# Kernel optimization log

Hardware: AMD Instinct MI355X
Metric: run time of the kernel (lower is better)

## Reference

```python
import jax, jax.numpy as jnp
import numpy as np

N, E, F, HID, HEADS, L, OUT = 25000, 400000, 128, 128, 2, 3, 10
C = HID // HEADS
EPS = 1e-5

def _ln(x, g, b):
    m = jnp.mean(x, -1, keepdims=True)
    v = jnp.mean((x - m) ** 2, -1, keepdims=True)
    return (x - m) / jnp.sqrt(v + EPS) * g + b

def _lrelu(x, s=0.01):
    return jnp.where(x >= 0, x, s * x)

def setup_inputs():
    key = jax.random.key(0)
    ks = iter(jax.random.split(key, 80))
    def nrm(shape, fan_in):
        return jax.random.normal(next(ks), shape, dtype=jnp.float32) / np.float32(np.sqrt(fan_in))
    return {
        "x": jax.random.normal(next(ks), (N, F), dtype=jnp.float32),
        "edge_index": jax.random.randint(next(ks), (2, E), 0, N, dtype=jnp.int32),
        "edge_attr": jax.random.uniform(next(ks), (E,), dtype=jnp.float32),
        "task_features": jax.random.normal(next(ks), (4,), dtype=jnp.float32),
        "emb_w": nrm((F, HID), F), "emb_b": jnp.zeros((HID,), jnp.float32),
        "emb_g": jnp.ones((HID,), jnp.float32), "emb_beta": jnp.zeros((HID,), jnp.float32),
        "gat_w": nrm((L, HID, HID), HID),
        "gat_as": nrm((L, HEADS, C), C), "gat_ad": nrm((L, HEADS, C), C),
        "gat_bias": jnp.zeros((L, HID), jnp.float32),
        "ec_w1": nrm((L, 2 * HID, HID), 2 * HID), "ec_b1": jnp.zeros((L, HID), jnp.float32),
        "ec_g1": jnp.ones((L, HID), jnp.float32), "ec_be1": jnp.zeros((L, HID), jnp.float32),
        "ec_w2": nrm((L, HID, HID), HID), "ec_b2": jnp.zeros((L, HID), jnp.float32),
        "ec_g2": jnp.ones((L, HID), jnp.float32), "ec_be2": jnp.zeros((L, HID), jnp.float32),
        "norm_g": jnp.ones((L, HID), jnp.float32), "norm_b": jnp.zeros((L, HID), jnp.float32),
        "task_w": nrm((4, HID), 4), "task_b": jnp.zeros((HID,), jnp.float32),
        "task_g": jnp.ones((HID,), jnp.float32), "task_beta": jnp.zeros((HID,), jnp.float32),
        "pa_w1": nrm((HID, HID // 2), HID), "pa_b1": jnp.zeros((HID // 2,), jnp.float32),
        "pa_w2": nrm((HID // 2, 1), HID // 2), "pa_b2": jnp.zeros((1,), jnp.float32),
        "v_w1": nrm((2 * HID, HID), 2 * HID), "v_b1": jnp.zeros((HID,), jnp.float32),
        "v_g": jnp.ones((HID,), jnp.float32), "v_be": jnp.zeros((HID,), jnp.float32),
        "v_w2": nrm((HID, 1), HID), "v_b2": jnp.zeros((1,), jnp.float32),
        "a_w1": nrm((2 * HID, HID), 2 * HID), "a_b1": jnp.zeros((HID,), jnp.float32),
        "a_g": jnp.ones((HID,), jnp.float32), "a_be": jnp.zeros((HID,), jnp.float32),
        "a_w2": nrm((HID, OUT), HID), "a_b2": jnp.zeros((OUT,), jnp.float32),
    }

def _forward(x, edge_attr, task_features, emb_w, emb_b, emb_g, emb_beta,
             gat_w, gat_as, gat_ad, gat_bias,
             ec_w1, ec_b1, ec_g1, ec_be1, ec_w2, ec_b2, ec_g2, ec_be2,
             norm_g, norm_b, task_w, task_b, task_g, task_beta,
             pa_w1, pa_b1, pa_w2, pa_b2,
             v_w1, v_b1, v_g, v_be, v_w2, v_b2,
             a_w1, a_b1, a_g, a_be, a_w2, a_b2, edge_index):
    src, dst = edge_index[0], edge_index[1]
    loop = jnp.arange(N, dtype=edge_index.dtype)
    src_sl = jnp.concatenate([src, loop])  # PyG GATConv adds self-loops
    dst_sl = jnp.concatenate([dst, loop])
    h = _lrelu(_ln(x @ emb_w + emb_b, emb_g, emb_beta))
    x0 = h
    for i in range(L):
        # --- GATConv (dropout inactive at eval) ---
        ht = (h @ gat_w[i]).reshape(N, HEADS, C)
        a_s = jnp.sum(ht * gat_as[i], -1)  # [N, HEADS]
        a_d = jnp.sum(ht * gat_ad[i], -1)
        e = _lrelu(a_s[src_sl] + a_d[dst_sl], 0.2)  # [E+N, HEADS]
        emax = jax.ops.segment_max(e, dst_sl, num_segments=N)
        ee = jnp.exp(e - emax[dst_sl])
        alpha = ee / jax.ops.segment_sum(ee, dst_sl, num_segments=N)[dst_sl]
        x1 = jax.ops.segment_sum(ht[src_sl] * alpha[:, :, None], dst_sl,
                                 num_segments=N).reshape(N, HID) + gat_bias[i]
        # --- EdgeConv: gather -> MLP -> weighted scatter-add ---
        ef = jnp.concatenate([h[src], h[dst]], axis=1)  # [E, 2*HID]
        ef = _lrelu(_ln(ef @ ec_w1[i] + ec_b1[i], ec_g1[i], ec_be1[i]), 0.2)
        ef = _lrelu(_ln(ef @ ec_w2[i] + ec_b2[i], ec_g2[i], ec_be2[i]), 0.2)
        ef = ef * edge_attr[:, None]
        x2 = jax.ops.segment_sum(ef, dst, num_segments=N)
        h = _lrelu(_ln(x1 + x2, norm_g[i], norm_b[i]))
        if i > 0:
            h = h + x0
            x0 = h
    # attention pooling over all nodes (batch=None path)
    w = jax.nn.softmax((_lrelu(h @ pa_w1 + pa_b1) @ pa_w2 + pa_b2)[:, 0])
    gf = jnp.sum(h * w[:, None], axis=0)  # [HID]
    te = _lrelu(_ln(task_features @ task_w + task_b, task_g, task_beta))
    cf = jnp.concatenate([gf, te], -1)  # [2*HID]
    value = _lrelu(_ln(cf @ v_w1 + v_b1, v_g, v_be)) @ v_w2 + v_b2
    adv = _lrelu(_ln(cf @ a_w1 + a_b1, a_g, a_be)) @ a_w2 + a_b2
    return value + (adv - jnp.mean(adv, -1, keepdims=True))

def reference(x, edge_index, edge_attr, task_features, emb_w, emb_b, emb_g, emb_beta, gat_w, gat_as, gat_ad, gat_bias, ec_w1, ec_b1, ec_g1, ec_be1, ec_w2, ec_b2, ec_g2, ec_be2, norm_g, norm_b, task_w, task_b, task_g, task_beta, pa_w1, pa_b1, pa_w2, pa_b2, v_w1, v_b1, v_g, v_be, v_w2, v_b2, a_w1, a_b1, a_g, a_be, a_w2, a_b2):
    return _forward(x, edge_attr, task_features, emb_w, emb_b, emb_g, emb_beta, gat_w, gat_as, gat_ad, gat_bias, ec_w1, ec_b1, ec_g1, ec_be1, ec_w2, ec_b2, ec_g2, ec_be2, norm_g, norm_b, task_w, task_b, task_g, task_beta, pa_w1, pa_b1, pa_w2, pa_b2, v_w1, v_b1, v_g, v_be, v_w2, v_b2, a_w1, a_b1, a_g, a_be, a_w2, a_b2, edge_index)
```

## Files before the change

### kernel.cpp

```cpp
#include <hip/hip_runtime.h>
#include <math.h>

#define NN 25000
#define EE 400000
#define LL 3
#define LNEPS 1e-5f
#define EB 64

typedef __attribute__((ext_vector_type(8))) short short8;
typedef __attribute__((ext_vector_type(16))) float f32x16;

__device__ __forceinline__ float lrelu(float x, float s) { return fmaxf(x, x * s); }

__device__ __forceinline__ unsigned int pack_bf2(float lo, float hi) {
    unsigned int ul = __float_as_uint(lo), uh = __float_as_uint(hi);
    ul = (ul + 0x7FFFu + ((ul >> 16) & 1u)) >> 16;
    uh = (uh + 0x7FFFu + ((uh >> 16) & 1u)) >> 16;
    return (uh << 16) | (ul & 0xFFFFu);
}
__device__ __forceinline__ float bf_lo(unsigned int u) { return __uint_as_float(u << 16); }
__device__ __forceinline__ float bf_hi(unsigned int u) { return __uint_as_float(u & 0xFFFF0000u); }

__device__ __forceinline__ void ln_stats128(float v, float* red, float& mean, float& inv) {
    float sm = v, sq = v * v;
#pragma unroll
    for (int m = 32; m >= 1; m >>= 1) { sm += __shfl_xor(sm, m); sq += __shfl_xor(sq, m); }
    __syncthreads();
    if ((threadIdx.x & 63) == 0) { red[(threadIdx.x >> 6) * 2] = sm; red[(threadIdx.x >> 6) * 2 + 1] = sq; }
    __syncthreads();
    sm = red[0] + red[2]; sq = red[1] + red[3];
    mean = sm * (1.f / 128.f);
    float var = sq * (1.f / 128.f) - mean * mean;
    inv = rsqrtf(var + LNEPS);
}

__global__ void k_hist(const int* __restrict__ dst, int* __restrict__ cnt, int ne)
{
    int i = blockIdx.x * 256 + threadIdx.x;
    if (i < ne) atomicAdd(&cnt[dst[i]], 1);
}

__global__ __launch_bounds__(1024) void k_scan(const int* __restrict__ cnt,
                                               int* __restrict__ starts, int n)
{
    __shared__ int tot[1024];
    int t = threadIdx.x;
    const int PER = (n + 1023) >> 10;
    int i0 = t * PER;
    int s = 0;
    for (int k = 0; k < PER; ++k) { int i = i0 + k; s += (i < n) ? cnt[i] : 0; }
    tot[t] = s;
    __syncthreads();
    for (int off = 1; off < 1024; off <<= 1) {
        int x = (t >= off) ? tot[t - off] : 0;
        __syncthreads();
        tot[t] += x;
        __syncthreads();
    }
    int run = (t > 0) ? tot[t - 1] : 0;
    for (int k = 0; k < PER; ++k) {
        int i = i0 + k;
        if (i < n) { starts[i] = run; run += cnt[i]; }
    }
    if (t == 1023) starts[n] = tot[1023];
}

__global__ void k_scatter(const int* __restrict__ src, const int* __restrict__ dst,
                          const float* __restrict__ ea, int* __restrict__ cursor,
                          int* __restrict__ s_src, int* __restrict__ s_dst,
                          float* __restrict__ s_ea, int ne)
{
    int i = blockIdx.x * 256 + threadIdx.x;
    if (i >= ne) return;
    int d = dst[i];
    int pos = atomicAdd(&cursor[d], 1);
    s_src[pos] = src[i];
    s_dst[pos] = d;
    s_ea[pos] = ea[i];
}

__global__ void k_prep(const float* __restrict__ gat_w, const float* __restrict__ ec_w1,
                       const float* __restrict__ ec_w2, const float* __restrict__ emb_w,
                       uint4* __restrict__ wf)
{
    int g = blockIdx.x * 256 + threadIdx.x;
    int m = g >> 11, f = g & 2047;
    const float* srcm;
    if (m < 3) srcm = gat_w + (size_t)m * 16384;
    else if (m < 9) { int t2 = m - 3; srcm = ec_w1 + (size_t)(t2 >> 1) * 32768 + (size_t)(t2 & 1) * 16384; }
    else if (m < 12) srcm = ec_w2 + (size_t)(m - 9) * 16384;
    else srcm = emb_w;
    int l = f & 63, ks = (f >> 6) & 7, nb = f >> 9;
    int k0 = ks * 16 + (l >> 5) * 8, col = nb * 32 + (l & 31);
    const float* wp = srcm + (size_t)k0 * 128 + col;
    uint4 r;
    r.x = pack_bf2(wp[0],   wp[128]);
    r.y = pack_bf2(wp[256], wp[384]);
    r.z = pack_bf2(wp[512], wp[640]);
    r.w = pack_bf2(wp[768], wp[896]);
    wf[g] = r;
}

__global__ __launch_bounds__(256) void k_emb(
    const float* __restrict__ in, const uint4* __restrict__ wfm,
    const float* __restrict__ bias, const float* __restrict__ g,
    const float* __restrict__ be, float* __restrict__ h,
    float* __restrict__ x0, int nrows)
{
    __shared__ __align__(16) unsigned int sA[64 * 64];
    __shared__ __align__(16) unsigned int sW[2048 * 4];
    float* sU = (float*)sW;
    const int tid = threadIdx.x;
    const int r0 = blockIdx.x * 64;
    {
        int row = tid >> 2, q = tid & 3;
        const float* srcp = in + (size_t)(r0 + row) * 128 + q * 32;
        bool ok = (r0 + row) < nrows;
#pragma unroll
        for (int i = 0; i < 8; ++i) {
            float4 v = ok ? *(const float4*)&srcp[i * 4] : make_float4(0.f, 0.f, 0.f, 0.f);
            int cu = (q * 16 + i * 2) ^ ((row & 15) << 2);
            *(uint2*)&sA[row * 64 + cu] = make_uint2(pack_bf2(v.x, v.y), pack_bf2(v.z, v.w));
        }
    }
    {
        uint4* sW4 = (uint4*)sW;
#pragma unroll
        for (int i = 0; i < 8; ++i) sW4[tid + 256 * i] = wfm[tid + 256 * i];
    }
    __syncthreads();
    const int w = tid >> 6, l = tid & 63;
    const int m0 = (w >> 1) * 32, nhalf = (w & 1);
    f32x16 acc0 = {}, acc1 = {};
#pragma unroll
    for (int ks = 0; ks < 8; ++ks) {
        int rw = m0 + (l & 31);
        int cu = (ks * 8 + (l >> 5) * 4) ^ ((rw & 15) << 2);
        short8 a = *(const short8*)&sA[rw * 64 + cu];
        short8 b0 = *(const short8*)&sW[((nhalf * 16 + ks) * 64 + l) * 4];
        short8 b1 = *(const short8*)&sW[(((nhalf * 2 + 1) * 8 + ks) * 64 + l) * 4];
        acc0 = __builtin_amdgcn_mfma_f32_32x32x16_bf16(a, b0, acc0, 0, 0, 0);
        acc1 = __builtin_amdgcn_mfma_f32_32x32x16_bf16(a, b1, acc1, 0, 0, 0);
    }
    __syncthreads();
    {
        int colbase = nhalf * 64 + (l & 31);
        float bb0 = bias[colbase], bb1 = bias[colbase + 32];
#pragma unroll
        for (int r = 0; r < 16; ++r) {
            int rw = m0 + (r & 3) + 8 * (r >> 2) + 4 * (l >> 5);
            sU[rw * 128 + colbase]      = acc0[r] + bb0;
            sU[rw * 128 + colbase + 32] = acc1[r] + bb1;
        }
    }
    __syncthreads();
    float2 gv = *(const float2*)&g[l * 2];
    float2 bv = *(const float2*)&be[l * 2];
    for (int it = 0; it < 16; ++it) {
        int rw = w * 16 + it;
        int grow = r0 + rw;
        if (grow >= nrows) break;
        float2 v = *(const float2*)&sU[rw * 128 + l * 2];
        float sm = v.x + v.y, sq = v.x * v.x + v.y * v.y;
#pragma unroll
        for (int m = 32; m >= 1; m >>= 1) { sm += __shfl_xor(sm, m); sq += __shfl_xor(sq, m); }
        float mean = sm * (1.f / 128.f);
        float var = sq * (1.f / 128.f) - mean * mean;
        float inv = rsqrtf(var + LNEPS);
        float o0 = lrelu((v.x - mean) * inv * gv.x + bv.x, 0.01f);
        float o1 = lrelu((v.y - mean) * inv * gv.y + bv.y, 0.01f);
        unsigned off = (unsigned)grow * 128u + (unsigned)(l * 2);
        *(float2*)&h[off]  = make_float2(o0, o1);
        *(float2*)&x0[off] = make_float2(o0, o1);
    }
}

__global__ __launch_bounds__(256) void k_gemm3(
    const float* __restrict__ in, const uint4* __restrict__ wf,
    int mht, int mA, int mB, const float* __restrict__ bA,
    unsigned* __restrict__ o0, unsigned* __restrict__ o1, unsigned* __restrict__ o2,
    int nrows)
{
    __shared__ __align__(16) unsigned int sA[64 * 64];
    __shared__ __align__(16) unsigned int sW[2048 * 4];
    const int tid = threadIdx.x;
    const int r0 = blockIdx.x * 64;
    {
        int row = tid >> 2, q = tid & 3;
        const float* srcp = in + (size_t)(r0 + row) * 128 + q * 32;
        bool ok = (r0 + row) < nrows;
#pragma unroll
        for (int i = 0; i < 8; ++i) {
            float4 v = ok ? *(const float4*)&srcp[i * 4] : make_float4(0.f, 0.f, 0.f, 0.f);
            unsigned int p0 = pack_bf2(v.x, v.y), p1 = pack_bf2(v.z, v.w);
            int cu = (q * 16 + i * 2) ^ ((row & 15) << 2);
            *(uint2*)&sA[row * 64 + cu] = make_uint2(p0, p1);
        }
    }
    __syncthreads();
    const int w = tid >> 6, l = tid & 63;
    const int m0 = (w >> 1) * 32, nhalf = (w & 1);
    short8 af[8];
#pragma unroll
    for (int ks = 0; ks < 8; ++ks) {
        int row = m0 + (l & 31);
        int cu = (ks * 8 + (l >> 5) * 4) ^ ((row & 15) << 2);
        af[ks] = *(const short8*)&sA[row * 64 + cu];
    }
    const int c = l & 31;
    const bool evenl = (c & 1) == 0;
    const unsigned uidx = (unsigned)(nhalf * 32 + (evenl ? (c >> 1) : (16 + (c >> 1))));
    auto do_mat = [&](int mat, unsigned* out, const float* bp) {
        __syncthreads();
        {
            const uint4* wsrc = wf + (size_t)mat * 2048;
            uint4* sW4 = (uint4*)sW;
#pragma unroll
            for (int i = 0; i < 8; ++i) sW4[tid + 256 * i] = wsrc[tid + 256 * i];
        }
        __syncthreads();
        f32x16 acc0 = {}, acc1 = {};
        const int nb0 = nhalf * 2;
#pragma unroll
        for (int ks = 0; ks < 8; ++ks) {
            short8 b0 = *(const short8*)&sW[((nb0 * 8 + ks) * 64 + l) * 4];
            short8 b1v = *(const short8*)&sW[(((nb0 + 1) * 8 + ks) * 64 + l) * 4];
            acc0 = __builtin_amdgcn_mfma_f32_32x32x16_bf16(af[ks], b0, acc0, 0, 0, 0);
            acc1 = __builtin_amdgcn_mfma_f32_32x32x16_bf16(af[ks], b1v, acc1, 0, 0, 0);
        }
        int colbase = nhalf * 64 + c;
        float badd0 = bp ? bp[colbase] : 0.f;
        float badd1 = bp ? bp[colbase + 32] : 0.f;
#pragma unroll
        for (int r = 0; r < 16; ++r) {
            float v0 = acc0[r] + badd0;
            float v1 = acc1[r] + badd1;
            float v0p = __shfl_xor(v0, 1);
            float v1p = __shfl_xor(v1, 1);
            int row = r0 + m0 + (r & 3) + 8 * (r >> 2) + 4 * (l >> 5);
            if (row < nrows) {
                unsigned val = evenl ? pack_bf2(v0, v0p) : pack_bf2(v1p, v1);
                out[(unsigned)row * 64u + uidx] = val;
            }
        }
    };
    do_mat(mht, o0, nullptr);
    do_mat(mA, o1, bA);
    do_mat(mB, o2, nullptr);
}

__global__ __launch_bounds__(512) void k_node_scores(
    const unsigned* __restrict__ htp, const unsigned* __restrict__ Apk,
    const unsigned* __restrict__ Bpk,
    const float* __restrict__ as_, const float* __restrict__ ad_,
    float* __restrict__ a_s, float* __restrict__ a_d,
    float* __restrict__ denom, float* __restrict__ selfe,
    float* __restrict__ rsA, float* __restrict__ rsB, int n)
{
    int wv = threadIdx.x >> 6, ln = threadIdx.x & 63;
    int node = blockIdx.x * 8 + wv;
    if (node >= n) return;
    unsigned off = (unsigned)node * 64u + (unsigned)ln;
    unsigned hv = htp[off], av = Apk[off], bv = Bpk[off];
    float h0 = bf_lo(hv), h1 = bf_hi(hv);
    float2 wsv = *(const float2*)&as_[ln * 2];
    float2 wdv = *(const float2*)&ad_[ln * 2];
    float ss = h0 * wsv.x + h1 * wsv.y;
    float sd = h0 * wdv.x + h1 * wdv.y;
    float sa = bf_lo(av) + bf_hi(av), sb = bf_lo(bv) + bf_hi(bv);
#pragma unroll
    for (int m = 16; m >= 1; m >>= 1) {
        ss += __shfl_xor(ss, m); sd += __shfl_xor(sd, m);
        sa += __shfl_xor(sa, m); sb += __shfl_xor(sb, m);
    }
    float sa2 = sa + __shfl_xor(sa, 32);
    float sb2 = sb + __shfl_xor(sb, 32);
    if ((ln & 31) == 0) {
        int hd = ln >> 5;
        a_s[node * 2 + hd] = ss;
        a_d[node * 2 + hd] = sd;
        float ev = expf(lrelu(ss + sd, 0.2f));
        denom[node * 2 + hd] = ev;
        selfe[node * 2 + hd] = ev;
        if (hd == 0) { rsA[node] = sa2; rsB[node] = sb2; }
    }
}

__global__ void k_edge_denom2(const int* __restrict__ s_src, const int* __restrict__ s_dst,
                              const float* __restrict__ a_s, const float* __restrict__ a_d,
                              float* __restrict__ denom, float* __restrict__ expo,
                              float4* __restrict__ xz, int nz4, int ne)
{
    int gtid = blockIdx.x * 256 + threadIdx.x;
    for (int i = gtid; i < nz4; i += gridDim.x * 256)
        xz[i] = make_float4(0.f, 0.f, 0.f, 0.f);
    int base = gtid * 8;
    if (base >= ne) return;
    int curd = -1;
    float acc0 = 0.f, acc1 = 0.f;
    for (int k = 0; k < 8; ++k) {
        int e = base + k;
        if (e >= ne) break;
        int s = s_src[e], d = s_dst[e];
        float v0 = expf(lrelu(a_s[(unsigned)(s * 2)]     + a_d[(unsigned)(d * 2)],     0.2f));
        float v1 = expf(lrelu(a_s[(unsigned)(s * 2 + 1)] + a_d[(unsigned)(d * 2 + 1)], 0.2f));
        *(float2*)&expo[(unsigned)e * 2] = make_float2(v0, v1);
        if (d != curd) {
            if (curd >= 0) { atomicAdd(&denom[curd * 2], acc0); atomicAdd(&denom[curd * 2 + 1], acc1); }
            curd = d; acc0 = v0; acc1 = v1;
        } else { acc0 += v0; acc1 += v1; }
    }
    if (curd >= 0) { atomicAdd(&denom[curd * 2], acc0); atomicAdd(&denom[curd * 2 + 1], acc1); }
}

__global__ __launch_bounds__(512) void k_edge_main(
    const unsigned* __restrict__ Apk, const unsigned* __restrict__ Bpk,
    const unsigned* __restrict__ htp,
    const int* __restrict__ s_src, const int* __restrict__ s_dst,
    const float* __restrict__ s_ea,
    const float* __restrict__ expo, const float* __restrict__ denom,
    const uint4* __restrict__ w2f,
    const float* __restrict__ rsA, const float* __restrict__ rsB,
    const float* __restrict__ g1, const float* __restrict__ be1,
    const float* __restrict__ b2, const float* __restrict__ g2, const float* __restrict__ be2,
    float* __restrict__ xsum, int ne)
{
    __shared__ __align__(16) unsigned int sWB[2048 * 4];
    __shared__ __align__(16) unsigned int sT32[EB * 64];
    __shared__ int   sS[EB], sD[EB];
    __shared__ float sEA[EB], sM[EB];
    __shared__ float sAl[EB * 2];
    __shared__ float sMean[EB], sInv[EB];
    __shared__ float sG1[128], sE1[128], sB2[128], sG2[128], sE2[128];
    float* sU = (float*)sWB;

    const int tid = threadIdx.x;
    {
        uint4* sWB4 = (uint4*)sWB;
#pragma unroll
        for (int i = 0; i < 4; ++i) { int f = tid + 512 * i; sWB4[f] = w2f[f]; }
    }
    if (tid < 128) {
        sG1[tid] = g1[tid]; sE1[tid] = be1[tid];
        sB2[tid] = b2[tid]; sG2[tid] = g2[tid]; sE2[tid] = be2[tid];
    }
    const int e0 = blockIdx.x * EB;
    const int nev = (ne - e0 < EB) ? (ne - e0) : EB;
    if (tid < EB) {
        if (tid < nev) {
            int s = s_src[e0 + tid], d = s_dst[e0 + tid];
            sS[tid] = s; sD[tid] = d; sEA[tid] = s_ea[e0 + tid];
            sM[tid] = (rsA[s] + rsB[d]) * (1.f / 128.f);
        } else { sS[tid] = 0; sD[tid] = -1; sEA[tid] = 0.f; sM[tid] = 0.f; }
    }
    if (tid < 2 * EB) {
        int le = tid >> 1, hd = tid & 1;
        float al = 0.f;
        if (le < nev) {
            int e = e0 + le;
            int d = s_dst[e];
            al = expo[(unsigned)e * 2 + hd] / denom[(unsigned)(d * 2 + hd)];
        }
        sAl[le * 2 + hd] = al;
    }
    __syncthreads();

    const int wv = tid >> 6, ln = tid & 63;
    const int half = ln >> 5, lc = ln & 31;

    {
        const float g10 = sG1[lc * 4], g11 = sG1[lc * 4 + 1], g12 = sG1[lc * 4 + 2], g13 = sG1[lc * 4 + 3];
        const float e10 = sE1[lc * 4], e11 = sE1[lc * 4 + 1], e12 = sE1[lc * 4 + 2], e13 = sE1[lc * 4 + 3];
        for (int j = 0; j < 4; ++j) {
            int e = wv * 8 + j * 2 + half;
            if (e < nev) {
                unsigned s = (unsigned)sS[e], d = (unsigned)sD[e];
                float mean = sM[e];
                uint2 av = *(const uint2*)&Apk[s * 64u + (unsigned)(lc * 2)];
                uint2 bv = *(const uint2*)&Bpk[d * 64u + (unsigned)(lc * 2)];
                float v0 = bf_lo(av.x) + bf_lo(bv.x) - mean;
                float v1 = bf_hi(av.x) + bf_hi(bv.x) - mean;
                float v2 = bf_lo(av.y) + bf_lo(bv.y) - mean;
                float v3 = bf_hi(av.y) + bf_hi(bv.y) - mean;
                float sq = v0 * v0 + v1 * v1 + v2 * v2 + v3 * v3;
#pragma unroll
                for (int m = 16; m >= 1; m >>= 1) sq += __shfl_xor(sq, m);
                float inv = rsqrtf(sq * (1.f / 128.f) + LNEPS);
                float t0 = lrelu(v0 * inv * g10 + e10, 0.2f);
                float t1 = lrelu(v1 * inv * g11 + e11, 0.2f);
                float t2 = lrelu(v2 * inv * g12 + e12, 0.2f);
                float t3 = lrelu(v3 * inv * g13 + e13, 0.2f);
                int cu = (lc * 2) ^ ((e & 15) << 2);
                *(uint2*)&sT32[e * 64 + cu] = make_uint2(pack_bf2(t0, t1), pack_bf2(t2, t3));
            }
        }
    }
    __syncthreads();

    {
        const int w = wv, l = ln;
        const int m0 = (w >> 2) * 32, n0 = (w & 3) * 32;
        f32x16 acc = {};
#pragma unroll
        for (int ks = 0; ks < 8; ++ks) {
            int row = m0 + (l & 31);
            int colu = (ks * 8 + (l >> 5) * 4) ^ ((row & 15) << 2);
            short8 a = *(const short8*)&sT32[row * 64 + colu];
            short8 b = *(const short8*)&sWB[((((w & 3) * 8 + ks) * 64 + l)) * 4];
            acc = __builtin_amdgcn_mfma_f32_32x32x16_bf16(a, b, acc, 0, 0, 0);
        }
        __syncthreads();
        float b2c = sB2[n0 + (l & 31)];
#pragma unroll
        for (int r = 0; r < 16; ++r) {
            int row = m0 + (r & 3) + 8 * (r >> 2) + 4 * (l >> 5);
            sU[row * 128 + n0 + (l & 31)] = acc[r] + b2c;
        }
    }
    __syncthreads();

    for (int j = 0; j < 4; ++j) {
        int e = wv * 8 + j * 2 + half;
        if (e < nev) {
            float4 u = *(const float4*)&sU[e * 128 + lc * 4];
            float sm = u.x + u.y + u.z + u.w;
            float sq = u.x * u.x + u.y * u.y + u.z * u.z + u.w * u.w;
#pragma unroll
            for (int m = 16; m >= 1; m >>= 1) { sm += __shfl_xor(sm, m); sq += __shfl_xor(sq, m); }
            if (lc == 0) {
                float mean = sm * (1.f / 128.f);
                sMean[e] = mean;
                sInv[e] = rsqrtf(sq * (1.f / 128.f) - mean * mean + LNEPS);
            }
        }
    }

    {
        const unsigned ln2 = (unsigned)(ln * 2);
        const float g2a = sG2[ln * 2], g2b = sG2[ln * 2 + 1];
        const float e2a = sE2[ln * 2], e2b = sE2[ln * 2 + 1];
        int curd = -1;
        float acc0 = 0.f, acc1 = 0.f;
        for (int j = 0; j < 8; ++j) {
            int e = wv * 8 + j;
            if (e >= nev) break;
            unsigned s = (unsigned)sS[e];
            int d = sD[e];
            float mean = sMean[e], inv = sInv[e];
            float2 uv = *(const float2*)&sU[e * 128 + ln * 2];
            float eav = sEA[e];
            float v0 = lrelu((uv.x - mean) * inv * g2a + e2a, 0.2f) * eav;
            float v1 = lrelu((uv.y - mean) * inv * g2b + e2b, 0.2f) * eav;
            float al = sAl[e * 2 + half];
            unsigned hv = htp[s * 64u + ln];
            v0 += bf_lo(hv) * al;
            v1 += bf_hi(hv) * al;
            if (d != curd) {
                if (curd >= 0) {
                    atomicAdd(&xsum[(unsigned)curd * 128u + ln2], acc0);
                    atomicAdd(&xsum[(unsigned)curd * 128u + ln2 + 1], acc1);
                }
                curd = d; acc0 = v0; acc1 = v1;
            } else { acc0 += v0; acc1 += v1; }
        }
        if (curd >= 0) {
            atomicAdd(&xsum[(unsigned)curd * 128u + ln2], acc0);
            atomicAdd(&xsum[(unsigned)curd * 128u + ln2 + 1], acc1);
        }
    }
}

__global__ __launch_bounds__(512) void k_norm8(const float* __restrict__ xsum,
                                               const unsigned* __restrict__ htp,
                                               const float* __restrict__ selfe,
                                               const float* __restrict__ denom,
                                               const float* __restrict__ gbias,
                                               const float* __restrict__ g,
                                               const float* __restrict__ b,
                                               float* __restrict__ x0,
                                               float* __restrict__ h, int n, int layer)
{
    int wv = threadIdx.x >> 6, ln = threadIdx.x & 63;
    int node = blockIdx.x * 8 + wv;
    if (node >= n) return;
    unsigned off = (unsigned)node * 128u + (unsigned)(ln * 2);
    int hd = ln >> 5;
    float alpha = selfe[node * 2 + hd] / denom[node * 2 + hd];
    unsigned hv = htp[(unsigned)node * 64u + (unsigned)ln];
    float2 gb = *(const float2*)&gbias[ln * 2];
    float2 v = *(const float2*)&xsum[off];
    v.x += gb.x + bf_lo(hv) * alpha;
    v.y += gb.y + bf_hi(hv) * alpha;
    float sm = v.x + v.y, sq = v.x * v.x + v.y * v.y;
#pragma unroll
    for (int m = 32; m >= 1; m >>= 1) { sm += __shfl_xor(sm, m); sq += __shfl_xor(sq, m); }
    float mean = sm * (1.f / 128.f);
    float var = sq * (1.f / 128.f) - mean * mean;
    float inv = rsqrtf(var + LNEPS);
    float2 gv = *(const float2*)&g[ln * 2];
    float2 bv = *(const float2*)&b[ln * 2];
    float val0 = lrelu((v.x - mean) * inv * gv.x + bv.x, 0.01f);
    float val1 = lrelu((v.y - mean) * inv * gv.y + bv.y, 0.01f);
    if (layer > 0) {
        float2 x0v = *(const float2*)&x0[off];
        val0 += x0v.x; val1 += x0v.y;
        *(float2*)&x0[off] = make_float2(val0, val1);
    }
    *(float2*)&h[off] = make_float2(val0, val1);
}

__global__ __launch_bounds__(256) void k_pool_score(const float* __restrict__ h,
    const float* __restrict__ w1, const float* __restrict__ b1,
    const float* __restrict__ w2, const float* __restrict__ b2,
    float* __restrict__ score, int n)
{
    int wv = threadIdx.x >> 6, ln = threadIdx.x & 63;
    int node = blockIdx.x * 4 + wv;
    if (node >= n) return;
    float acc = b1[ln];
    const float* hr = h + (size_t)node * 128;
    for (int k = 0; k < 128; ++k) acc += hr[k] * w1[k * 64 + ln];
    acc = lrelu(acc, 0.01f) * w2[ln];
#pragma unroll
    for (int m = 32; m >= 1; m >>= 1) acc += __shfl_xor(acc, m);
    if (ln == 0) score[node] = acc + b2[0];
}

__global__ __launch_bounds__(256) void k_softmax_reduce(const float* __restrict__ score,
                                                        float* __restrict__ stats,
                                                        float* __restrict__ gf, int n)
{
    __shared__ float red[8];
    int t = threadIdx.x;
    float mx = -1e30f;
    for (int i = t; i < n; i += 256) mx = fmaxf(mx, score[i]);
#pragma unroll
    for (int m = 32; m >= 1; m >>= 1) mx = fmaxf(mx, __shfl_xor(mx, m));
    if ((t & 63) == 0) red[t >> 6] = mx;
    __syncthreads();
    mx = fmaxf(fmaxf(red[0], red[1]), fmaxf(red[2], red[3]));
    float s = 0.f;
    for (int i = t; i < n; i += 256) s += expf(score[i] - mx);
#pragma unroll
    for (int m = 32; m >= 1; m >>= 1) s += __shfl_xor(s, m);
    if ((t & 63) == 0) red[4 + (t >> 6)] = s;
    __syncthreads();
    s = red[4] + red[5] + red[6] + red[7];
    if (t == 0) { stats[0] = mx; stats[1] = s; }
    if (t < 128) gf[t] = 0.f;
}

__global__ __launch_bounds__(128) void k_gf(const float* __restrict__ h,
                                            const float* __restrict__ score,
                                            const float* __restrict__ stats,
                                            float* __restrict__ gf, int n)
{
    int c = threadIdx.x;
    float mx = stats[0], invZ = 1.f / stats[1];
    int per = (n + gridDim.x - 1) / gridDim.x;
    int n0 = blockIdx.x * per;
    int n1 = n0 + per; if (n1 > n) n1 = n;
    float acc = 0.f;
    for (int i = n0; i < n1; ++i)
        acc += expf(score[i] - mx) * invZ * h[(size_t)i * 128 + c];
    atomicAdd(&gf[c], acc);
}

__global__ __launch_bounds__(128) void k_head(
    const float* __restrict__ gf, const float* __restrict__ tf,
    const float* __restrict__ task_w, const float* __restrict__ task_b,
    const float* __restrict__ task_g, const float* __restrict__ task_be,
    const float* __restrict__ v_w1, const float* __restrict__ v_b1,
    const float* __restrict__ v_g, const float* __restrict__ v_be,
    const float* __restrict__ v_w2, const float* __restrict__ v_b2,
    const float* __restrict__ a_w1, const float* __restrict__ a_b1,
    const float* __restrict__ a_g, const float* __restrict__ a_be,
    const float* __restrict__ a_w2, const float* __restrict__ a_b2,
    float* __restrict__ out)
{
    __shared__ float cf[256], hbuf[128], red[4], sc[2], adv[10];
    int t = threadIdx.x;
    float mean, inv;
    float te = task_b[t];
#pragma unroll
    for (int k = 0; k < 4; ++k) te += tf[k] * task_w[k * 128 + t];
    ln_stats128(te, red, mean, inv);
    te = lrelu((te - mean) * inv * task_g[t] + task_be[t], 0.01f);
    cf[t] = gf[t]; cf[128 + t] = te;
    __syncthreads();
    float v = v_b1[t];
    for (int k = 0; k < 256; ++k) v += cf[k] * v_w1[k * 128 + t];
    ln_stats128(v, red, mean, inv);
    v = lrelu((v - mean) * inv * v_g[t] + v_be[t], 0.01f);
    float pv = v * v_w2[t];
#pragma unroll
    for (int m = 32; m >= 1; m >>= 1) pv += __shfl_xor(pv, m);
    __syncthreads();
    if ((t & 63) == 0) red[t >> 6] = pv;
    __syncthreads();
    if (t == 0) sc[0] = red[0] + red[1] + v_b2[0];
    float a = a_b1[t];
    for (int k = 0; k < 256; ++k) a += cf[k] * a_w1[k * 128 + t];
    ln_stats128(a, red, mean, inv);
    a = lrelu((a - mean) * inv * a_g[t] + a_be[t], 0.01f);
    hbuf[t] = a;
    __syncthreads();
    if (t < 10) {
        float s = a_b2[t];
        for (int c = 0; c < 128; ++c) s += hbuf[c] * a_w2[c * 10 + t];
        adv[t] = s;
    }
    __syncthreads();
    if (t == 0) {
        float m10 = 0.f;
        for (int o = 0; o < 10; ++o) m10 += adv[o];
        sc[1] = m10 * 0.1f;
    }
    __syncthreads();
    if (t < 10) out[t] = sc[0] + adv[t] - sc[1];
}

extern "C" void kernel_launch(void* const* d_in, const int* in_sizes, int n_in,
                              void* d_out, int out_size, void* d_ws, size_t ws_size,
                              hipStream_t stream)
{
    const float* x        = (const float*)d_in[0];
    const int*   ei       = (const int*)d_in[1];
    const float* ea       = (const float*)d_in[2];
    const float* tf       = (const float*)d_in[3];
    const float* emb_w    = (const float*)d_in[4];
    const float* emb_b    = (const float*)d_in[5];
    const float* emb_g    = (const float*)d_in[6];
    const float* emb_beta = (const float*)d_in[7];
    const float* gat_w    = (const float*)d_in[8];
    const float* gat_as   = (const float*)d_in[9];
    const float* gat_ad   = (const float*)d_in[10];
    const float* gat_bias = (const float*)d_in[11];
    const float* ec_w1    = (const float*)d_in[12];
    const float* ec_b1    = (const float*)d_in[13];
    const float* ec_g1    = (const float*)d_in[14];
    const float* ec_be1   = (const float*)d_in[15];
    const float* ec_w2    = (const float*)d_in[16];
    const float* ec_b2    = (const float*)d_in[17];
    const float* ec_g2    = (const float*)d_in[18];
    const float* ec_be2   = (const float*)d_in[19];
    const float* norm_g   = (const float*)d_in[20];
    const float* norm_b   = (const float*)d_in[21];
    const float* task_w   = (const float*)d_in[22];
    const float* task_b   = (const float*)d_in[23];
    const float* task_g   = (const float*)d_in[24];
    const float* task_be  = (const float*)d_in[25];
    const float* pa_w1    = (const float*)d_in[26];
    const float* pa_b1    = (const float*)d_in[27];
    const float* pa_w2    = (const float*)d_in[28];
    const float* pa_b2    = (const float*)d_in[29];
    const float* v_w1     = (const float*)d_in[30];
    const float* v_b1     = (const float*)d_in[31];
    const float* v_g      = (const float*)d_in[32];
    const float* v_be     = (const float*)d_in[33];
    const float* v_w2     = (const float*)d_in[34];
    const float* v_b2     = (const float*)d_in[35];
    const float* a_w1     = (const float*)d_in[36];
    const float* a_b1     = (const float*)d_in[37];
    const float* a_g      = (const float*)d_in[38];
    const float* a_be     = (const float*)d_in[39];
    const float* a_w2     = (const float*)d_in[40];
    const float* a_b2     = (const float*)d_in[41];

    const int n = in_sizes[0] / 128;
    const int e = in_sizes[2];
    const int* src = ei;
    const int* dst = ei + e;

    float* ws = (float*)d_ws;
    uint4* wf = (uint4*)ws;
    float* base = ws + 13 * 2048 * 4;
    const size_t NR = (size_t)n * 128;
    const size_t NP = (size_t)n * 64;
    float* h    = base;
    float* x0   = base + NR;
    float* xs   = base + 2 * NR;
    unsigned* htp = (unsigned*)(base + 3 * NR);
    unsigned* Apk = htp + NP;
    unsigned* Bpk = Apk + NP;
    float* a_s  = (float*)(Bpk + NP);
    float* a_d  = a_s + (size_t)n * 2;
    float* den  = a_d + (size_t)n * 2;
    float* selfe = den + (size_t)n * 2;
    float* rsA  = selfe + (size_t)n * 2;
    float* rsB  = rsA + n;
    float* score = rsB + n;
    float* stats = score + n;
    float* gf    = stats + 2;
    int*   cnt    = (int*)(gf + 128);
    int*   starts = cnt + n;
    int*   s_src  = starts + (n + 1);
    int*   s_dst  = s_src + e;
    float* s_ea   = (float*)(s_dst + e);
    float* expo   = s_ea + e;

    const int ng64 = (n + 63) / 64;
    const int ng8 = (n + 7) / 8;
    const int ngd = ((e + 7) / 8 + 255) / 256;

    hipMemsetAsync(cnt, 0, (size_t)n * sizeof(int), stream);
    k_hist<<<(e + 255) / 256, 256, 0, stream>>>(dst, cnt, e);
    k_scan<<<1, 1024, 0, stream>>>(cnt, starts, n);
    hipMemcpyAsync(cnt, starts, (size_t)n * sizeof(int), hipMemcpyDeviceToDevice, stream);
    k_scatter<<<(e + 255) / 256, 256, 0, stream>>>(src, dst, ea, cnt, s_src, s_dst, s_ea, e);
    k_prep<<<104, 256, 0, stream>>>(gat_w, ec_w1, ec_w2, emb_w, wf);

    k_emb<<<ng64, 256, 0, stream>>>(x, wf + (size_t)12 * 2048, emb_b, emb_g, emb_beta, h, x0, n);

    for (int i = 0; i < LL; ++i) {
        k_gemm3<<<ng64, 256, 0, stream>>>(h, wf, i, 3 + 2 * i, 4 + 2 * i,
                                          ec_b1 + i * 128, htp, Apk, Bpk, n);
        k_node_scores<<<ng8, 512, 0, stream>>>(htp, Apk, Bpk, gat_as + i * 128, gat_ad + i * 128,
                                               a_s, a_d, den, selfe, rsA, rsB, n);
        k_edge_denom2<<<ngd, 256, 0, stream>>>(s_src, s_dst, a_s, a_d, den, expo,
                                               (float4*)xs, n * 32, e);
        k_edge_main<<<(e + EB - 1) / EB, 512, 0, stream>>>(Apk, Bpk, htp, s_src, s_dst, s_ea,
                                                           expo, den,
                                                           wf + (size_t)(9 + i) * 2048,
                                                           rsA, rsB,
                                                           ec_g1 + i * 128, ec_be1 + i * 128,
                                                           ec_b2 + i * 128, ec_g2 + i * 128, ec_be2 + i * 128,
                                                           xs, e);
        k_norm8<<<ng8, 512, 0, stream>>>(xs, htp, selfe, den, gat_bias + i * 128,
                                         norm_g + i * 128, norm_b + i * 128, x0, h, n, i);
    }

    k_pool_score<<<(n + 3) / 4, 256, 0, stream>>>(h, pa_w1, pa_b1, pa_w2, pa_b2, score, n);
    k_softmax_reduce<<<1, 256, 0, stream>>>(score, stats, gf, n);
    k_gf<<<200, 128, 0, stream>>>(h, score, stats, gf, n);
    k_head<<<1, 128, 0, stream>>>(gf, tf, task_w, task_b, task_g, task_be,
                                  v_w1, v_b1, v_g, v_be, v_w2, v_b2,
                                  a_w1, a_b1, a_g, a_be, a_w2, a_b2,
                                  (float*)d_out);
}
```

Baseline: 717.4 us.

## Widen gemm3 blocks, halve edge-denom work per thread, fuse LN2 stats into scatter

After: 1.162 ms. 1.62x slower.

```diff
diff --git a/kernel.cpp b/kernel.cpp
--- a/kernel.cpp
+++ b/kernel.cpp
@@ -175,7 +175,7 @@
     }
 }
 
-__global__ __launch_bounds__(256) void k_gemm3(
+__global__ __launch_bounds__(512) void k_gemm3(
     const float* __restrict__ in, const uint4* __restrict__ wf,
     int mht, int mA, int mB, const float* __restrict__ bA,
     unsigned* __restrict__ o0, unsigned* __restrict__ o1, unsigned* __restrict__ o2,
@@ -186,62 +186,47 @@
     const int tid = threadIdx.x;
     const int r0 = blockIdx.x * 64;
     {
-        int row = tid >> 2, q = tid & 3;
-        const float* srcp = in + (size_t)(r0 + row) * 128 + q * 32;
+        int row = tid >> 3, q = tid & 7;
+        const float* srcp = in + (size_t)(r0 + row) * 128 + q * 16;
         bool ok = (r0 + row) < nrows;
 #pragma unroll
-        for (int i = 0; i < 8; ++i) {
+        for (int i = 0; i < 4; ++i) {
             float4 v = ok ? *(const float4*)&srcp[i * 4] : make_float4(0.f, 0.f, 0.f, 0.f);
-            unsigned int p0 = pack_bf2(v.x, v.y), p1 = pack_bf2(v.z, v.w);
-            int cu = (q * 16 + i * 2) ^ ((row & 15) << 2);
-            *(uint2*)&sA[row * 64 + cu] = make_uint2(p0, p1);
+            int cu = (q * 8 + i * 2) ^ ((row & 15) << 2);
+            *(uint2*)&sA[row * 64 + cu] = make_uint2(pack_bf2(v.x, v.y), pack_bf2(v.z, v.w));
         }
     }
     __syncthreads();
     const int w = tid >> 6, l = tid & 63;
-    const int m0 = (w >> 1) * 32, nhalf = (w & 1);
-    short8 af[8];
-#pragma unroll
-    for (int ks = 0; ks < 8; ++ks) {
-        int row = m0 + (l & 31);
-        int cu = (ks * 8 + (l >> 5) * 4) ^ ((row & 15) << 2);
-        af[ks] = *(const short8*)&sA[row * 64 + cu];
-    }
+    const int mr = w >> 2, nq = w & 3;
     const int c = l & 31;
-    const bool evenl = (c & 1) == 0;
-    const unsigned uidx = (unsigned)(nhalf * 32 + (evenl ? (c >> 1) : (16 + (c >> 1))));
+    const bool evenc = (c & 1) == 0;
     auto do_mat = [&](int mat, unsigned* out, const float* bp) {
         __syncthreads();
         {
             const uint4* wsrc = wf + (size_t)mat * 2048;
             uint4* sW4 = (uint4*)sW;
 #pragma unroll
-            for (int i = 0; i < 8; ++i) sW4[tid + 256 * i] = wsrc[tid + 256 * i];
+            for (int i = 0; i < 4; ++i) sW4[tid + 512 * i] = wsrc[tid + 512 * i];
         }
         __syncthreads();
-        f32x16 acc0 = {}, acc1 = {};
-        const int nb0 = nhalf * 2;
+        f32x16 acc = {};
 #pragma unroll
         for (int ks = 0; ks < 8; ++ks) {
-            short8 b0 = *(const short8*)&sW[((nb0 * 8 + ks) * 64 + l) * 4];
-            short8 b1v = *(const short8*)&sW[(((nb0 + 1) * 8 + ks) * 64 + l) * 4];
-            acc0 = __builtin_amdgcn_mfma_f32_32x32x16_bf16(af[ks], b0, acc0, 0, 0, 0);
-            acc1 = __builtin_amdgcn_mfma_f32_32x32x16_bf16(af[ks], b1v, acc1, 0, 0, 0);
-        }
-        int colbase = nhalf * 64 + c;
-        float badd0 = bp ? bp[colbase] : 0.f;
-        float badd1 = bp ? bp[colbase + 32] : 0.f;
+            int row = mr * 32 + c;
+            int cu = (ks * 8 + (l >> 5) * 4) ^ ((row & 15) << 2);
+            short8 a = *(const short8*)&sA[row * 64 + cu];
+            short8 b = *(const short8*)&sW[((nq * 8 + ks) * 64 + l) * 4];
+            acc = __builtin_amdgcn_mfma_f32_32x32x16_bf16(a, b, acc, 0, 0, 0);
+        }
+        float badd = bp ? bp[nq * 32 + c] : 0.f;
 #pragma unroll
         for (int r = 0; r < 16; ++r) {
-            float v0 = acc0[r] + badd0;
-            float v1 = acc1[r] + badd1;
-            float v0p = __shfl_xor(v0, 1);
-            float v1p = __shfl_xor(v1, 1);
-            int row = r0 + m0 + (r & 3) + 8 * (r >> 2) + 4 * (l >> 5);
-            if (row < nrows) {
-                unsigned val = evenl ? pack_bf2(v0, v0p) : pack_bf2(v1p, v1);
-                out[(unsigned)row * 64u + uidx] = val;
-            }
+            float v = acc[r] + badd;
+            float vp = __shfl_xor(v, 1);
+            int row = r0 + mr * 32 + (r & 3) + 8 * (r >> 2) + 4 * (l >> 5);
+            if (evenc && row < nrows)
+                out[(unsigned)row * 64u + (unsigned)(nq * 16 + (c >> 1))] = pack_bf2(v, vp);
         }
     };
     do_mat(mht, o0, nullptr);
@@ -294,11 +279,11 @@
     int gtid = blockIdx.x * 256 + threadIdx.x;
     for (int i = gtid; i < nz4; i += gridDim.x * 256)
         xz[i] = make_float4(0.f, 0.f, 0.f, 0.f);
-    int base = gtid * 8;
+    int base = gtid * 4;
     if (base >= ne) return;
     int curd = -1;
     float acc0 = 0.f, acc1 = 0.f;
-    for (int k = 0; k < 8; ++k) {
+    for (int k = 0; k < 4; ++k) {
         int e = base + k;
         if (e >= ne) break;
         int s = s_src[e], d = s_dst[e];
@@ -330,7 +315,6 @@
     __shared__ int   sS[EB], sD[EB];
     __shared__ float sEA[EB], sM[EB];
     __shared__ float sAl[EB * 2];
-    __shared__ float sMean[EB], sInv[EB];
     __shared__ float sG1[128], sE1[128], sB2[128], sG2[128], sE2[128];
     float* sU = (float*)sWB;
 
@@ -419,53 +403,48 @@
     }
     __syncthreads();
 
-    for (int j = 0; j < 4; ++j) {
-        int e = wv * 8 + j * 2 + half;
-        if (e < nev) {
-            float4 u = *(const float4*)&sU[e * 128 + lc * 4];
-            float sm = u.x + u.y + u.z + u.w;
-            float sq = u.x * u.x + u.y * u.y + u.z * u.z + u.w * u.w;
-#pragma unroll
-            for (int m = 16; m >= 1; m >>= 1) { sm += __shfl_xor(sm, m); sq += __shfl_xor(sq, m); }
-            if (lc == 0) {
+    {
+        const float g20 = sG2[lc * 4], g21 = sG2[lc * 4 + 1], g22 = sG2[lc * 4 + 2], g23 = sG2[lc * 4 + 3];
+        const float e20 = sE2[lc * 4], e21 = sE2[lc * 4 + 1], e22 = sE2[lc * 4 + 2], e23 = sE2[lc * 4 + 3];
+        int curd = -1;
+        float a0 = 0.f, a1 = 0.f, a2 = 0.f, a3 = 0.f;
+        for (int j = 0; j < 4; ++j) {
+            int e = wv * 8 + half * 4 + j;
+            if (e < nev) {
+                unsigned s = (unsigned)sS[e];
+                int d = sD[e];
+                float4 u = *(const float4*)&sU[e * 128 + lc * 4];
+                float sm = u.x + u.y + u.z + u.w;
+                float sq = u.x * u.x + u.y * u.y + u.z * u.z + u.w * u.w;
+#pragma unroll
+                for (int m = 16; m >= 1; m >>= 1) { sm += __shfl_xor(sm, m); sq += __shfl_xor(sq, m); }
                 float mean = sm * (1.f / 128.f);
-                sMean[e] = mean;
-                sInv[e] = rsqrtf(sq * (1.f / 128.f) - mean * mean + LNEPS);
+                float inv = rsqrtf(sq * (1.f / 128.f) - mean * mean + LNEPS);
+                float eav = sEA[e];
+                float al = sAl[e * 2 + (lc >> 4)];
+                uint2 hv = *(const uint2*)&htp[s * 64u + (unsigned)(lc * 2)];
+                float v0 = lrelu((u.x - mean) * inv * g20 + e20, 0.2f) * eav + bf_lo(hv.x) * al;
+                float v1 = lrelu((u.y - mean) * inv * g21 + e21, 0.2f) * eav + bf_hi(hv.x) * al;
+                float v2 = lrelu((u.z - mean) * inv * g22 + e22, 0.2f) * eav + bf_lo(hv.y) * al;
+                float v3 = lrelu((u.w - mean) * inv * g23 + e23, 0.2f) * eav + bf_hi(hv.y) * al;
+                if (d != curd) {
+                    if (curd >= 0) {
+                        unsigned bo = (unsigned)curd * 128u + (unsigned)(lc * 4);
+                        atomicAdd(&xsum[bo], a0);
+                        atomicAdd(&xsum[bo + 1], a1);
+                        atomicAdd(&xsum[bo + 2], a2);
+                        atomicAdd(&xsum[bo + 3], a3);
+                    }
+                    curd = d; a0 = v0; a1 = v1; a2 = v2; a3 = v3;
+                } else { a0 += v0; a1 += v1; a2 += v2; a3 += v3; }
             }
         }
-    }
-
-    {
-        const unsigned ln2 = (unsigned)(ln * 2);
-        const float g2a = sG2[ln * 2], g2b = sG2[ln * 2 + 1];
-        const float e2a = sE2[ln * 2], e2b = sE2[ln * 2 + 1];
-        int curd = -1;
-        float acc0 = 0.f, acc1 = 0.f;
-        for (int j = 0; j < 8; ++j) {
-            int e = wv * 8 + j;
-            if (e >= nev) break;
-            unsigned s = (unsigned)sS[e];
-            int d = sD[e];
-            float mean = sMean[e], inv = sInv[e];
-            float2 uv = *(const float2*)&sU[e * 128 + ln * 2];
-            float eav = sEA[e];
-            float v0 = lrelu((uv.x - mean) * inv * g2a + e2a, 0.2f) * eav;
-            float v1 = lrelu((uv.y - mean) * inv * g2b + e2b, 0.2f) * eav;
-            float al = sAl[e * 2 + half];
-            unsigned hv = htp[s * 64u + ln];
-            v0 += bf_lo(hv) * al;
-            v1 += bf_hi(hv) * al;
-            if (d != curd) {
-                if (curd >= 0) {
-                    atomicAdd(&xsum[(unsigned)curd * 128u + ln2], acc0);
-                    atomicAdd(&xsum[(unsigned)curd * 128u + ln2 + 1], acc1);
-                }
-                curd = d; acc0 = v0; acc1 = v1;
-            } else { acc0 += v0; acc1 += v1; }
-        }
         if (curd >= 0) {
-            atomicAdd(&xsum[(unsigned)curd * 128u + ln2], acc0);
-            atomicAdd(&xsum[(unsigned)curd * 128u + ln2 + 1], acc1);
+            unsigned bo = (unsigned)curd * 128u + (unsigned)(lc * 4);
+            atomicAdd(&xsum[bo], a0);
+            atomicAdd(&xsum[bo + 1], a1);
+            atomicAdd(&xsum[bo + 2], a2);
+            atomicAdd(&xsum[bo + 3], a3);
         }
     }
 }
@@ -701,7 +680,7 @@
 
     const int ng64 = (n + 63) / 64;
     const int ng8 = (n + 7) / 8;
-    const int ngd = ((e + 7) / 8 + 255) / 256;
+    const int ngd = ((e + 3) / 4 + 255) / 256;
 
     hipMemsetAsync(cnt, 0, (size_t)n * sizeof(int), stream);
     k_hist<<<(e + 255) / 256, 256, 0, stream>>>(dst, cnt, e);
@@ -713,7 +692,7 @@
     k_emb<<<ng64, 256, 0, stream>>>(x, wf + (size_t)12 * 2048, emb_b, emb_g, emb_beta, h, x0, n);
 
     for (int i = 0; i < LL; ++i) {
-        k_gemm3<<<ng64, 256, 0, stream>>>(h, wf, i, 3 + 2 * i, 4 + 2 * i,
+        k_gemm3<<<ng64, 512, 0, stream>>>(h, wf, i, 3 + 2 * i, 4 + 2 * i,
                                           ec_b1 + i * 128, htp, Apk, Bpk, n);
         k_node_scores<<<ng8, 512, 0, stream>>>(htp, Apk, Bpk, gat_as + i * 128, gat_ad + i * 128,
                                                a_s, a_d, den, selfe, rsA, rsB, n);
```

## Fuse post-layer norm and residual into next layer's GEMM prologue

Applied to the files above, without the earlier changes.

Result: no change. 719.7 us (+0.3%).

```diff
diff --git a/kernel.cpp b/kernel.cpp
--- a/kernel.cpp
+++ b/kernel.cpp
@@ -176,10 +176,14 @@
 }
 
 __global__ __launch_bounds__(256) void k_gemm3(
-    const float* __restrict__ in, const uint4* __restrict__ wf,
+    const float* __restrict__ in, const unsigned* __restrict__ htp_in,
+    const float* __restrict__ selfe, const float* __restrict__ denom,
+    const float* __restrict__ gbias, const float* __restrict__ ng,
+    const float* __restrict__ nb, float* __restrict__ x0,
+    const uint4* __restrict__ wf,
     int mht, int mA, int mB, const float* __restrict__ bA,
     unsigned* __restrict__ o0, unsigned* __restrict__ o1, unsigned* __restrict__ o2,
-    int nrows)
+    int nrows, int mode)
 {
     __shared__ __align__(16) unsigned int sA[64 * 64];
     __shared__ __align__(16) unsigned int sW[2048 * 4];
@@ -187,14 +191,57 @@
     const int r0 = blockIdx.x * 64;
     {
         int row = tid >> 2, q = tid & 3;
-        const float* srcp = in + (size_t)(r0 + row) * 128 + q * 32;
-        bool ok = (r0 + row) < nrows;
-#pragma unroll
-        for (int i = 0; i < 8; ++i) {
-            float4 v = ok ? *(const float4*)&srcp[i * 4] : make_float4(0.f, 0.f, 0.f, 0.f);
-            unsigned int p0 = pack_bf2(v.x, v.y), p1 = pack_bf2(v.z, v.w);
-            int cu = (q * 16 + i * 2) ^ ((row & 15) << 2);
-            *(uint2*)&sA[row * 64 + cu] = make_uint2(p0, p1);
+        int node = r0 + row;
+        bool ok = node < nrows;
+        if (mode == 0) {
+            const float* srcp = in + (size_t)node * 128 + q * 32;
+#pragma unroll
+            for (int i = 0; i < 8; ++i) {
+                float4 v = ok ? *(const float4*)&srcp[i * 4] : make_float4(0.f, 0.f, 0.f, 0.f);
+                int cu = (q * 16 + i * 2) ^ ((row & 15) << 2);
+                *(uint2*)&sA[row * 64 + cu] = make_uint2(pack_bf2(v.x, v.y), pack_bf2(v.z, v.w));
+            }
+        } else {
+            unsigned off128 = (unsigned)node * 128u + (unsigned)(q * 32);
+            unsigned off64  = (unsigned)node * 64u + (unsigned)(q * 16);
+            int hd = q >> 1;
+            float alpha = ok ? (selfe[node * 2 + hd] / denom[node * 2 + hd]) : 0.f;
+            float4 vv[8];
+            float sm = 0.f, sq = 0.f;
+#pragma unroll
+            for (int i = 0; i < 8; ++i) {
+                float4 v = ok ? *(const float4*)&in[off128 + i * 4] : make_float4(0.f, 0.f, 0.f, 0.f);
+                uint2 hvp = ok ? *(const uint2*)&htp_in[off64 + i * 2] : make_uint2(0u, 0u);
+                float4 gbv = *(const float4*)&gbias[q * 32 + i * 4];
+                v.x += gbv.x + bf_lo(hvp.x) * alpha;
+                v.y += gbv.y + bf_hi(hvp.x) * alpha;
+                v.z += gbv.z + bf_lo(hvp.y) * alpha;
+                v.w += gbv.w + bf_hi(hvp.y) * alpha;
+                vv[i] = v;
+                sm += v.x + v.y + v.z + v.w;
+                sq += v.x * v.x + v.y * v.y + v.z * v.z + v.w * v.w;
+            }
+            sm += __shfl_xor(sm, 1); sq += __shfl_xor(sq, 1);
+            sm += __shfl_xor(sm, 2); sq += __shfl_xor(sq, 2);
+            float mean = sm * (1.f / 128.f);
+            float inv = rsqrtf(sq * (1.f / 128.f) - mean * mean + LNEPS);
+#pragma unroll
+            for (int i = 0; i < 8; ++i) {
+                float4 v = vv[i];
+                float4 gv = *(const float4*)&ng[q * 32 + i * 4];
+                float4 bv = *(const float4*)&nb[q * 32 + i * 4];
+                float w0 = lrelu((v.x - mean) * inv * gv.x + bv.x, 0.01f);
+                float w1 = lrelu((v.y - mean) * inv * gv.y + bv.y, 0.01f);
+                float w2 = lrelu((v.z - mean) * inv * gv.z + bv.z, 0.01f);
+                float w3 = lrelu((v.w - mean) * inv * gv.w + bv.w, 0.01f);
+                if (mode == 2 && ok) {
+                    float4 xv = *(const float4*)&x0[off128 + i * 4];
+                    w0 += xv.x; w1 += xv.y; w2 += xv.z; w3 += xv.w;
+                    *(float4*)&x0[off128 + i * 4] = make_float4(w0, w1, w2, w3);
+                }
+                int cu = (q * 16 + i * 2) ^ ((row & 15) << 2);
+                *(uint2*)&sA[row * 64 + cu] = make_uint2(pack_bf2(w0, w1), pack_bf2(w2, w3));
+            }
         }
     }
     __syncthreads();
@@ -713,8 +760,19 @@
     k_emb<<<ng64, 256, 0, stream>>>(x, wf + (size_t)12 * 2048, emb_b, emb_g, emb_beta, h, x0, n);
 
     for (int i = 0; i < LL; ++i) {
-        k_gemm3<<<ng64, 256, 0, stream>>>(h, wf, i, 3 + 2 * i, 4 + 2 * i,
-                                          ec_b1 + i * 128, htp, Apk, Bpk, n);
+        if (i == 0) {
+            k_gemm3<<<ng64, 256, 0, stream>>>(h, nullptr, nullptr, nullptr,
+                                              nullptr, nullptr, nullptr, nullptr,
+                                              wf, i, 3 + 2 * i, 4 + 2 * i,
+                                              ec_b1 + i * 128, htp, Apk, Bpk, n, 0);
+        } else {
+            k_gemm3<<<ng64, 256, 0, stream>>>(xs, htp, selfe, den,
+                                              gat_bias + (i - 1) * 128,
+                                              norm_g + (i - 1) * 128, norm_b + (i - 1) * 128, x0,
+                                              wf, i, 3 + 2 * i, 4 + 2 * i,
+                                              ec_b1 + i * 128, htp, Apk, Bpk, n,
+                                              (i == 2) ? 2 : 1);
+        }
         k_node_scores<<<ng8, 512, 0, stream>>>(htp, Apk, Bpk, gat_as + i * 128, gat_ad + i * 128,
                                                a_s, a_d, den, selfe, rsA, rsB, n);
         k_edge_denom2<<<ngd, 256, 0, stream>>>(s_src, s_dst, a_s, a_d, den, expo,
@@ -726,9 +784,9 @@
                                                            ec_g1 + i * 128, ec_be1 + i * 128,
                                                            ec_b2 + i * 128, ec_g2 + i * 128, ec_be2 + i * 128,
                                                            xs, e);
-        k_norm8<<<ng8, 512, 0, stream>>>(xs, htp, selfe, den, gat_bias + i * 128,
-                                         norm_g + i * 128, norm_b + i * 128, x0, h, n, i);
-    }
+    }
+    k_norm8<<<ng8, 512, 0, stream>>>(xs, htp, selfe, den, gat_bias + 2 * 128,
+                                     norm_g + 2 * 128, norm_b + 2 * 128, x0, h, n, 2);
 
     k_pool_score<<<(n + 3) / 4, 256, 0, stream>>>(h, pa_w1, pa_b1, pa_w2, pa_b2, score, n);
     k_softmax_reduce<<<1, 256, 0, stream>>>(score, stats, gf, n);
```
